# Optimization experiments

Measured on AMD Instinct MI355X. Metric: run time of the kernel, lower is better.

Reference implementation:

```python
import jax, jax.numpy as jnp
import numpy as np

B, S, D, U = 4, 2048, 1024, 1024

def setup_inputs() -> dict:
    key = jax.random.key(0)
    ks = jax.random.split(key, 6)
    glorot = lambda k, shape: jax.random.uniform(k, shape, jnp.float32,
                                                 -np.sqrt(6.0/(shape[0]+shape[1])),
                                                 np.sqrt(6.0/(shape[0]+shape[1])))
    return {
        "inputs": jax.random.normal(ks[0], (B, S, D), jnp.float32),
        "Wq": glorot(ks[1], (D, U)),
        "Wk": glorot(ks[2], (D, U)),
        "Wv": glorot(ks[3], (D, U)),
        "Wo": glorot(ks[4], (U, D)),
        "bo": jnp.zeros((D,), jnp.float32),
        "scale": jnp.asarray(1.0 / np.sqrt(U), jnp.float32),
    }

def reference(inputs, Wq, Wk, Wv, Wo, bo, scale):
    # q, k, v: [B, S, U]
    q = jnp.einsum('bsd,du->bsu', inputs, Wq)
    k = jnp.einsum('bsd,du->bsu', inputs, Wk)
    v = jnp.einsum('bsd,du->bsu', inputs, Wv)
    # scores: [B, S, S]
    scores = jnp.einsum('bqu,bku->bqk', q, k) * scale
    weights = jax.nn.softmax(scores, axis=-1)
    context = jnp.einsum('bqk,bku->bqu', weights, v)
    output = jnp.einsum('bsu,ud->bsd', context, Wo) + bo
    return (output, weights)
```

## Files before the change

### kernel.cpp

```cpp
#include <hip/hip_runtime.h>
#include <hip/hip_bf16.h>

#define BB 4
#define SS 2048
#define DD 1024
#define UU 1024
#define NTOK (BB*SS)

typedef unsigned short ushort_t;
typedef __attribute__((ext_vector_type(8))) short bf16x8;
typedef __attribute__((ext_vector_type(4))) float f32x4;
typedef __attribute__((ext_vector_type(4))) unsigned short u16x4;

__device__ inline unsigned short f2bf(float f) {
  unsigned u = __builtin_bit_cast(unsigned, f);
  u += 0x7FFFu + ((u >> 16) & 1u);
  return (unsigned short)(u >> 16);
}

__device__ inline void gload_lds16(const ushort_t* g, ushort_t* l) {
  __builtin_amdgcn_global_load_lds(
      (const __attribute__((address_space(1))) void*)g,
      (__attribute__((address_space(3))) void*)l, 16, 0, 0);
}

#define WAIT_LGKM0 do { asm volatile("s_waitcnt lgkmcnt(0)" ::: "memory"); \
                        __builtin_amdgcn_sched_barrier(0); } while(0)
#define WAIT_VM(N) do { asm volatile("s_waitcnt vmcnt(" #N ")" ::: "memory"); \
                        __builtin_amdgcn_sched_barrier(0); } while(0)
#define BAR        do { __builtin_amdgcn_s_barrier(); \
                        __builtin_amdgcn_sched_barrier(0); } while(0)

__global__ __launch_bounds__(256) void cast_f32_bf16(const float* __restrict__ in,
                                                     ushort_t* __restrict__ out,
                                                     long n) {
  long i = ((long)blockIdx.x * blockDim.x + threadIdx.x) * 4;
  long stride = (long)gridDim.x * blockDim.x * 4;
  for (long idx = i; idx < n; idx += stride) {
    float4 v = *(const float4*)(in + idx);
    u16x4 o;
    o[0] = f2bf(v.x); o[1] = f2bf(v.y); o[2] = f2bf(v.z); o[3] = f2bf(v.w);
    *(u16x4*)(out + idx) = o;
  }
}

struct TPack { const float* s[4]; ushort_t* d[4]; };
__global__ __launch_bounds__(256) void transpose_cast_w4(TPack p) {
  __shared__ float tile[32][33];
  const float* in = p.s[blockIdx.z];
  ushort_t* out = p.d[blockIdx.z];
  int bx = blockIdx.x * 32, by = blockIdx.y * 32;
  int tx = threadIdx.x, ty = threadIdx.y;
  #pragma unroll
  for (int j = 0; j < 32; j += 8)
    tile[ty + j][tx] = in[(long)(by + ty + j) * 1024 + bx + tx];
  __syncthreads();
  #pragma unroll
  for (int j = 0; j < 32; j += 8)
    out[(long)(bx + ty + j) * 1024 + by + tx] = f2bf(tile[tx][ty + j]);
}

__global__ __launch_bounds__(256) void transpose_bf16_batched(const ushort_t* __restrict__ in,
                                                              ushort_t* __restrict__ out,
                                                              int R, int C) {
  __shared__ ushort_t tile[32][34];
  long z = (long)blockIdx.z * R * C;
  int bx = blockIdx.x * 32, by = blockIdx.y * 32;
  int tx = threadIdx.x, ty = threadIdx.y;
  #pragma unroll
  for (int j = 0; j < 32; j += 8)
    tile[ty + j][tx] = in[z + (long)(by + ty + j) * C + bx + tx];
  __syncthreads();
  #pragma unroll
  for (int j = 0; j < 32; j += 8)
    out[z + (long)(bx + ty + j) * R + by + tx] = tile[tx][ty + j];
}

template<int BN>
__global__ __launch_bounds__(512, 2) void gemm8p(
    const ushort_t* __restrict__ A,
    const ushort_t* __restrict__ Bt,
    float* __restrict__ Cf,
    ushort_t* __restrict__ Cb,
    const float* __restrict__ bias,
    const float* __restrict__ alpha_ptr,
    int M, int N, int K,
    long sA, long sB, long sC) {
  static_assert(BN == 128 || BN == 256, "BN");
  constexpr int NREP = BN / 64;
  constexpr int BSTEPS = BN / 64;
  __shared__ __align__(16) ushort_t As[2][256 * 64];
  __shared__ __align__(16) ushort_t Bs[2][BN * 64];

  const int tid = threadIdx.x;
  const int lane = tid & 63;
  const int wid = tid >> 6;
  const int wm = wid >> 2, wn = wid & 3;

  int bx = blockIdx.x, by = blockIdx.y, bz = blockIdx.z;
  {
    const int gx = gridDim.x, gy = gridDim.y, gz = gridDim.z;
    const int total = gx * gy * gz;
    const int ppx = total >> 3;
    if ((total & 7) == 0 && ppx % gx == 0) {
      const int lin = blockIdx.x + gx * (blockIdx.y + gy * blockIdx.z);
      const int xcd = lin & 7, i = lin >> 3;
      const int p = xcd * (ppx / gx) + i / gx;
      bx = i % gx; by = p % gy; bz = p / gy;
    }
  }

  const long zA = (long)bz * sA;
  const long zB = (long)bz * sB;
  const long zC = (long)bz * sC;
  const int m0 = by * 256;
  const int n0 = bx * BN;

  f32x4 acc[8][NREP] = {};

  const int srow = tid >> 3;
  const int cs = (tid & 7) ^ (srow & 7);
  const ushort_t* Aps = A + zA + (long)(m0 + srow) * K + cs * 8;
  const ushort_t* Bps = Bt + zB + (long)(n0 + srow) * K + cs * 8;
  const int ldst = wid * 512;

  const int rsel = (lane & 15);
  const int csel = (lane >> 4);
  const int cxor = (lane & 7);

  const int nt = K / 64;

  auto STAGE = [&](int tk, int b) {
    const long kof = (long)tk * 64;
    #pragma unroll
    for (int j = 0; j < BSTEPS; ++j)
      gload_lds16(Bps + (long)(j * 64) * K + kof, &Bs[b][j * 4096 + ldst]);
    gload_lds16(Aps + (long)(0 * 64) * K + kof, &As[b][0 * 4096 + ldst]);
    gload_lds16(Aps + (long)(2 * 64) * K + kof, &As[b][2 * 4096 + ldst]);
    gload_lds16(Aps + (long)(1 * 64) * K + kof, &As[b][1 * 4096 + ldst]);
    gload_lds16(Aps + (long)(3 * 64) * K + kof, &As[b][3 * 4096 + ldst]);
  };

  STAGE(0, 0);
  WAIT_VM(2);
  BAR;

  for (int t = 0; t < nt; ++t) {
    const int cur = t & 1, nxt = cur ^ 1;
    const bool pf = (t + 1 < nt);
    const ushort_t* __restrict__ Ac = &As[cur][0];
    const ushort_t* __restrict__ Bc = &Bs[cur][0];

    bf16x8 bfr[NREP][2], af[4][2];

    #pragma unroll
    for (int n = 0; n < NREP; ++n)
      #pragma unroll
      for (int kk = 0; kk < 2; ++kk)
        bfr[n][kk] = *(const bf16x8*)&Bc[(wn * (BN/4) + n * 16 + rsel) * 64
                                         + ((kk * 4 + csel) ^ cxor) * 8];
    #pragma unroll
    for (int m = 0; m < 4; ++m)
      #pragma unroll
      for (int kk = 0; kk < 2; ++kk)
        af[m][kk] = *(const bf16x8*)&Ac[(wm * 128 + m * 16 + rsel) * 64
                                        + ((kk * 4 + csel) ^ cxor) * 8];
    if (pf) STAGE(t + 1, nxt);
    BAR;
    WAIT_LGKM0;
    __builtin_amdgcn_s_setprio(1);
    #pragma unroll
    for (int m = 0; m < 4; ++m)
      #pragma unroll
      for (int n = 0; n < (NREP == 4 ? 2 : NREP); ++n)
        #pragma unroll
        for (int kk = 0; kk < 2; ++kk)
          acc[m][n] = __builtin_amdgcn_mfma_f32_16x16x32_bf16(af[m][kk], bfr[n][kk], acc[m][n], 0, 0, 0);
    __builtin_amdgcn_s_setprio(0);
    BAR;

    if (NREP == 4) {
      __builtin_amdgcn_s_setprio(1);
      #pragma unroll
      for (int m = 0; m < 4; ++m)
        #pragma unroll
        for (int n = 2; n < 4; ++n)
          #pragma unroll
          for (int kk = 0; kk < 2; ++kk)
            acc[m][n] = __builtin_amdgcn_mfma_f32_16x16x32_bf16(af[m][kk], bfr[n][kk], acc[m][n], 0, 0, 0);
      __builtin_amdgcn_s_setprio(0);
      if (pf) { WAIT_VM(8); } else { WAIT_VM(0); }
      BAR;

      #pragma unroll
      for (int m = 0; m < 4; ++m)
        #pragma unroll
        for (int kk = 0; kk < 2; ++kk)
          af[m][kk] = *(const bf16x8*)&Ac[(wm * 128 + 64 + m * 16 + rsel) * 64
                                          + ((kk * 4 + csel) ^ cxor) * 8];
      BAR;
      WAIT_LGKM0;
      __builtin_amdgcn_s_setprio(1);
      #pragma unroll
      for (int m = 0; m < 4; ++m)
        #pragma unroll
        for (int n = 0; n < 2; ++n)
          #pragma unroll
          for (int kk = 0; kk < 2; ++kk)
            acc[m + 4][n] = __builtin_amdgcn_mfma_f32_16x16x32_bf16(af[m][kk], bfr[n][kk], acc[m + 4][n], 0, 0, 0);
      __builtin_amdgcn_s_setprio(0);
      BAR;

      __builtin_amdgcn_s_setprio(1);
      #pragma unroll
      for (int m = 0; m < 4; ++m)
        #pragma unroll
        for (int n = 2; n < 4; ++n)
          #pragma unroll
          for (int kk = 0; kk < 2; ++kk)
            acc[m + 4][n] = __builtin_amdgcn_mfma_f32_16x16x32_bf16(af[m][kk], bfr[n][kk], acc[m + 4][n], 0, 0, 0);
      __builtin_amdgcn_s_setprio(0);
      if (pf) { WAIT_VM(2); }
      BAR;
    } else {
      if (pf) { WAIT_VM(6); } else { WAIT_VM(0); }
      BAR;

      #pragma unroll
      for (int m = 0; m < 4; ++m)
        #pragma unroll
        for (int kk = 0; kk < 2; ++kk)
          af[m][kk] = *(const bf16x8*)&Ac[(wm * 128 + 64 + m * 16 + rsel) * 64
                                          + ((kk * 4 + csel) ^ cxor) * 8];
      BAR;
      WAIT_LGKM0;
      __builtin_amdgcn_s_setprio(1);
      #pragma unroll
      for (int m = 0; m < 4; ++m)
        #pragma unroll
        for (int n = 0; n < NREP; ++n)
          #pragma unroll
          for (int kk = 0; kk < 2; ++kk)
            acc[m + 4][n] = __builtin_amdgcn_mfma_f32_16x16x32_bf16(af[m][kk], bfr[n][kk], acc[m + 4][n], 0, 0, 0);
      __builtin_amdgcn_s_setprio(0);
      if (pf) { WAIT_VM(2); }
      BAR;
    }
  }

  const float alpha = alpha_ptr ? *alpha_ptr : 1.0f;
  const int crow0 = m0 + wm * 128 + csel * 4;
  const int ccol0 = n0 + wn * (BN / 4) + rsel;
  #pragma unroll
  for (int m = 0; m < 8; ++m) {
    #pragma unroll
    for (int n = 0; n < NREP; ++n) {
      const int cc = ccol0 + n * 16;
      const float bv = bias ? bias[cc] : 0.0f;
      #pragma unroll
      for (int r = 0; r < 4; ++r) {
        const int rr = crow0 + m * 16 + r;
        const float v = acc[m][n][r] * alpha + bv;
        const long idx = zC + (long)rr * N + cc;
        if (Cf) Cf[idx] = v;
        if (Cb) Cb[idx] = f2bf(v);
      }
    }
  }
}

__global__ __launch_bounds__(256) void softmax_rows(float* __restrict__ Wf,
                                                    ushort_t* __restrict__ Pb) {
  const int t = threadIdx.x;
  const int lane = t & 63, wid = t >> 6;
  const long base = (long)blockIdx.x * SS;
  float* p = Wf + base;

  float4 a = *(const float4*)(p + t * 4);
  float4 b = *(const float4*)(p + 1024 + t * 4);

  float m = fmaxf(fmaxf(fmaxf(a.x, a.y), fmaxf(a.z, a.w)),
                  fmaxf(fmaxf(b.x, b.y), fmaxf(b.z, b.w)));
  #pragma unroll
  for (int off = 32; off; off >>= 1) m = fmaxf(m, __shfl_xor(m, off));
  __shared__ float redm[4];
  __shared__ float reds[4];
  if (lane == 0) redm[wid] = m;
  __syncthreads();
  m = fmaxf(fmaxf(redm[0], redm[1]), fmaxf(redm[2], redm[3]));

  float e[8];
  e[0] = __expf(a.x - m); e[1] = __expf(a.y - m); e[2] = __expf(a.z - m); e[3] = __expf(a.w - m);
  e[4] = __expf(b.x - m); e[5] = __expf(b.y - m); e[6] = __expf(b.z - m); e[7] = __expf(b.w - m);
  float s = (e[0] + e[1]) + (e[2] + e[3]) + (e[4] + e[5]) + (e[6] + e[7]);
  #pragma unroll
  for (int off = 32; off; off >>= 1) s += __shfl_xor(s, off);
  if (lane == 0) reds[wid] = s;
  __syncthreads();
  s = (reds[0] + reds[1]) + (reds[2] + reds[3]);
  const float inv = 1.0f / s;

  float4 oa = make_float4(e[0] * inv, e[1] * inv, e[2] * inv, e[3] * inv);
  float4 ob = make_float4(e[4] * inv, e[5] * inv, e[6] * inv, e[7] * inv);
  *(float4*)(p + t * 4) = oa;
  *(float4*)(p + 1024 + t * 4) = ob;

  u16x4 ba, bb2;
  ba[0] = f2bf(oa.x); ba[1] = f2bf(oa.y); ba[2] = f2bf(oa.z); ba[3] = f2bf(oa.w);
  bb2[0] = f2bf(ob.x); bb2[1] = f2bf(ob.y); bb2[2] = f2bf(ob.z); bb2[3] = f2bf(ob.w);
  *(u16x4*)(Pb + base + t * 4) = ba;
  *(u16x4*)(Pb + base + 1024 + t * 4) = bb2;
}

extern "C" void kernel_launch(void* const* d_in, const int* in_sizes, int n_in,
                              void* d_out, int out_size, void* d_ws, size_t ws_size,
                              hipStream_t stream) {
  const float* X     = (const float*)d_in[0];
  const float* Wq    = (const float*)d_in[1];
  const float* Wk    = (const float*)d_in[2];
  const float* Wv    = (const float*)d_in[3];
  const float* Wo    = (const float*)d_in[4];
  const float* bo    = (const float*)d_in[5];
  const float* scale = (const float*)d_in[6];

  float* out = (float*)d_out;
  float* wts = out + (long)NTOK * DD;

  ushort_t* ws = (ushort_t*)d_ws;
  ushort_t* Xb  = ws;
  ushort_t* Qb  = Xb + (long)NTOK * DD;
  ushort_t* Kb  = Qb + (long)NTOK * UU;
  ushort_t* Vb  = Kb + (long)NTOK * UU;
  ushort_t* Wqt = Vb + (long)NTOK * UU;
  ushort_t* Wkt = Wqt + (long)UU * DD;
  ushort_t* Wvt = Wkt + (long)UU * DD;
  ushort_t* Wot = Wvt + (long)UU * DD;
  ushort_t* Cb  = Xb;
  ushort_t* Vt  = Qb;
  ushort_t* Pb  = Kb;

  cast_f32_bf16<<<2048, 256, 0, stream>>>(X, Xb, (long)NTOK * DD);

  TPack tp;
  tp.s[0] = Wq; tp.s[1] = Wk; tp.s[2] = Wv; tp.s[3] = Wo;
  tp.d[0] = Wqt; tp.d[1] = Wkt; tp.d[2] = Wvt; tp.d[3] = Wot;
  transpose_cast_w4<<<dim3(32, 32, 4), dim3(32, 8), 0, stream>>>(tp);

  dim3 gProj(UU/128, NTOK/256, 3);
  gemm8p<128><<<gProj, 512, 0, stream>>>(Xb, Wqt, nullptr, Qb, nullptr, nullptr,
                                         NTOK, UU, DD,
                                         0, (long)UU * DD, (long)NTOK * UU);

  dim3 gScores(SS/256, SS/256, BB);
  gemm8p<256><<<gScores, 512, 0, stream>>>(Qb, Kb, wts, nullptr, nullptr, scale,
                                           SS, SS, UU,
                                           (long)SS * UU, (long)SS * UU, (long)SS * SS);

  transpose_bf16_batched<<<dim3(UU/32, SS/32, BB), dim3(32, 8), 0, stream>>>(Vb, Vt, SS, UU);

  softmax_rows<<<BB * SS, 256, 0, stream>>>(wts, Pb);

  dim3 gPV(UU/128, SS/256, BB);
  gemm8p<128><<<gPV, 512, 0, stream>>>(Pb, Vt, nullptr, Cb, nullptr, nullptr,
                                       SS, UU, SS,
                                       (long)SS * SS, (long)UU * SS, (long)SS * UU);

  dim3 gOut(DD/128, NTOK/256, 1);
  gemm8p<128><<<gOut, 512, 0, stream>>>(Cb, Wot, out, nullptr, bo, nullptr,
                                        NTOK, DD, UU, 0, 0, 0);
}
```

Before: 361.1 us.

## Split GEMM into 256x256 and 128x256 kernels with two-tile unrolled pipelines

Replaces the templated GEMM with two kernels. One is a 256x256 kernel that processes two K-tiles per iteration and staggers A and B prefetches across the compute phases. The other is a 128x256 kernel with a triple-buffered B tile in LDS. The projection GEMM moves to 256-wide N tiles, and the PV and output GEMMs move to 128x256 tiles. The goal is to overlap global-to-LDS loads with MFMA phases more finely and to raise data reuse, at the cost of more LDS per block and more complex waitcnt accounting that could race if the counts are wrong.

```diff
diff --git a/kernel.cpp b/kernel.cpp
--- a/kernel.cpp
+++ b/kernel.cpp
@@ -26,10 +26,14 @@
 
 #define WAIT_LGKM0 do { asm volatile("s_waitcnt lgkmcnt(0)" ::: "memory"); \
                         __builtin_amdgcn_sched_barrier(0); } while(0)
+#define WAIT_LGKM(N) do { asm volatile("s_waitcnt lgkmcnt(" #N ")" ::: "memory"); \
+                        __builtin_amdgcn_sched_barrier(0); } while(0)
 #define WAIT_VM(N) do { asm volatile("s_waitcnt vmcnt(" #N ")" ::: "memory"); \
                         __builtin_amdgcn_sched_barrier(0); } while(0)
 #define BAR        do { __builtin_amdgcn_s_barrier(); \
                         __builtin_amdgcn_sched_barrier(0); } while(0)
+#define PRIO1      __builtin_amdgcn_s_setprio(1)
+#define PRIO0      __builtin_amdgcn_s_setprio(0)
 
 __global__ __launch_bounds__(256) void cast_f32_bf16(const float* __restrict__ in,
                                                      ushort_t* __restrict__ out,
@@ -76,8 +80,27 @@
     out[z + (long)(bx + ty + j) * R + by + tx] = tile[tx][ty + j];
 }
 
-template<int BN>
-__global__ __launch_bounds__(512, 2) void gemm8p(
+#define RD_A(Ax, MB) do { \
+  _Pragma("unroll") for (int m = 0; m < 4; ++m) \
+    _Pragma("unroll") for (int kk = 0; kk < 2; ++kk) \
+      af[m][kk] = *(const bf16x8*)&(Ax)[((MB) + m * 16 + rsel) * 64 \
+                                        + ((kk * 4 + csel) ^ cxor) * 8]; \
+} while(0)
+#define RD_B(Bx, NH) do { \
+  _Pragma("unroll") for (int n = 0; n < 2; ++n) \
+    _Pragma("unroll") for (int kk = 0; kk < 2; ++kk) \
+      bfr[(NH)*2 + n][kk] = *(const bf16x8*)&(Bx)[(wn * 64 + ((NH)*2 + n) * 16 + rsel) * 64 \
+                                                  + ((kk * 4 + csel) ^ cxor) * 8]; \
+} while(0)
+#define MM16(MH, NH) do { \
+  _Pragma("unroll") for (int m = 0; m < 4; ++m) \
+    _Pragma("unroll") for (int n = 0; n < 2; ++n) \
+      _Pragma("unroll") for (int kk = 0; kk < 2; ++kk) \
+        acc[(MH)*4 + m][(NH)*2 + n] = __builtin_amdgcn_mfma_f32_16x16x32_bf16( \
+            af[m][kk], bfr[(NH)*2 + n][kk], acc[(MH)*4 + m][(NH)*2 + n], 0, 0, 0); \
+} while(0)
+
+__global__ __launch_bounds__(512, 2) void gemm256_8p(
     const ushort_t* __restrict__ A,
     const ushort_t* __restrict__ Bt,
     float* __restrict__ Cf,
@@ -86,11 +109,8 @@
     const float* __restrict__ alpha_ptr,
     int M, int N, int K,
     long sA, long sB, long sC) {
-  static_assert(BN == 128 || BN == 256, "BN");
-  constexpr int NREP = BN / 64;
-  constexpr int BSTEPS = BN / 64;
   __shared__ __align__(16) ushort_t As[2][256 * 64];
-  __shared__ __align__(16) ushort_t Bs[2][BN * 64];
+  __shared__ __align__(16) ushort_t Bs[2][256 * 64];
 
   const int tid = threadIdx.x;
   const int lane = tid & 63;
@@ -114,9 +134,9 @@
   const long zB = (long)bz * sB;
   const long zC = (long)bz * sC;
   const int m0 = by * 256;
-  const int n0 = bx * BN;
-
-  f32x4 acc[8][NREP] = {};
+  const int n0 = bx * 256;
+
+  f32x4 acc[8][4] = {};
 
   const int srow = tid >> 3;
   const int cs = (tid & 7) ^ (srow & 7);
@@ -129,132 +149,89 @@
   const int cxor = (lane & 7);
 
   const int nt = K / 64;
-
-  auto STAGE = [&](int tk, int b) {
-    const long kof = (long)tk * 64;
-    #pragma unroll
-    for (int j = 0; j < BSTEPS; ++j)
-      gload_lds16(Bps + (long)(j * 64) * K + kof, &Bs[b][j * 4096 + ldst]);
-    gload_lds16(Aps + (long)(0 * 64) * K + kof, &As[b][0 * 4096 + ldst]);
-    gload_lds16(Aps + (long)(2 * 64) * K + kof, &As[b][2 * 4096 + ldst]);
-    gload_lds16(Aps + (long)(1 * 64) * K + kof, &As[b][1 * 4096 + ldst]);
-    gload_lds16(Aps + (long)(3 * 64) * K + kof, &As[b][3 * 4096 + ldst]);
-  };
-
-  STAGE(0, 0);
-  WAIT_VM(2);
+  const int nIter = nt / 2;
+
+  #define STA256(tk, g) gload_lds16(Aps + (long)((g) * 64) * K + (long)(tk) * 64, \
+                                    &As[(tk) & 1][(g) * 4096 + ldst])
+  #define STB256(tk, g) gload_lds16(Bps + (long)((g) * 64) * K + (long)(tk) * 64, \
+                                    &Bs[(tk) & 1][(g) * 4096 + ldst])
+
+  STB256(0, 0); STB256(0, 1); STB256(0, 2); STB256(0, 3);
+  STA256(0, 0); STA256(0, 1); STA256(0, 2); STA256(0, 3);
+  STB256(1, 0); STB256(1, 1); STB256(1, 2); STB256(1, 3);
+  WAIT_VM(4);
   BAR;
 
-  for (int t = 0; t < nt; ++t) {
-    const int cur = t & 1, nxt = cur ^ 1;
-    const bool pf = (t + 1 < nt);
-    const ushort_t* __restrict__ Ac = &As[cur][0];
-    const ushort_t* __restrict__ Bc = &Bs[cur][0];
-
-    bf16x8 bfr[NREP][2], af[4][2];
-
-    #pragma unroll
-    for (int n = 0; n < NREP; ++n)
-      #pragma unroll
-      for (int kk = 0; kk < 2; ++kk)
-        bfr[n][kk] = *(const bf16x8*)&Bc[(wn * (BN/4) + n * 16 + rsel) * 64
-                                         + ((kk * 4 + csel) ^ cxor) * 8];
-    #pragma unroll
-    for (int m = 0; m < 4; ++m)
-      #pragma unroll
-      for (int kk = 0; kk < 2; ++kk)
-        af[m][kk] = *(const bf16x8*)&Ac[(wm * 128 + m * 16 + rsel) * 64
-                                        + ((kk * 4 + csel) ^ cxor) * 8];
-    if (pf) STAGE(t + 1, nxt);
-    BAR;
-    WAIT_LGKM0;
-    __builtin_amdgcn_s_setprio(1);
-    #pragma unroll
-    for (int m = 0; m < 4; ++m)
-      #pragma unroll
-      for (int n = 0; n < (NREP == 4 ? 2 : NREP); ++n)
-        #pragma unroll
-        for (int kk = 0; kk < 2; ++kk)
-          acc[m][n] = __builtin_amdgcn_mfma_f32_16x16x32_bf16(af[m][kk], bfr[n][kk], acc[m][n], 0, 0, 0);
-    __builtin_amdgcn_s_setprio(0);
-    BAR;
-
-    if (NREP == 4) {
-      __builtin_amdgcn_s_setprio(1);
-      #pragma unroll
-      for (int m = 0; m < 4; ++m)
-        #pragma unroll
-        for (int n = 2; n < 4; ++n)
-          #pragma unroll
-          for (int kk = 0; kk < 2; ++kk)
-            acc[m][n] = __builtin_amdgcn_mfma_f32_16x16x32_bf16(af[m][kk], bfr[n][kk], acc[m][n], 0, 0, 0);
-      __builtin_amdgcn_s_setprio(0);
-      if (pf) { WAIT_VM(8); } else { WAIT_VM(0); }
-      BAR;
-
-      #pragma unroll
-      for (int m = 0; m < 4; ++m)
-        #pragma unroll
-        for (int kk = 0; kk < 2; ++kk)
-          af[m][kk] = *(const bf16x8*)&Ac[(wm * 128 + 64 + m * 16 + rsel) * 64
-                                          + ((kk * 4 + csel) ^ cxor) * 8];
-      BAR;
-      WAIT_LGKM0;
-      __builtin_amdgcn_s_setprio(1);
-      #pragma unroll
-      for (int m = 0; m < 4; ++m)
-        #pragma unroll
-        for (int n = 0; n < 2; ++n)
-          #pragma unroll
-          for (int kk = 0; kk < 2; ++kk)
-            acc[m + 4][n] = __builtin_amdgcn_mfma_f32_16x16x32_bf16(af[m][kk], bfr[n][kk], acc[m + 4][n], 0, 0, 0);
-      __builtin_amdgcn_s_setprio(0);
-      BAR;
-
-      __builtin_amdgcn_s_setprio(1);
-      #pragma unroll
-      for (int m = 0; m < 4; ++m)
-        #pragma unroll
-        for (int n = 2; n < 4; ++n)
-          #pragma unroll
-          for (int kk = 0; kk < 2; ++kk)
-            acc[m + 4][n] = __builtin_amdgcn_mfma_f32_16x16x32_bf16(af[m][kk], bfr[n][kk], acc[m + 4][n], 0, 0, 0);
-      __builtin_amdgcn_s_setprio(0);
-      if (pf) { WAIT_VM(2); }
-      BAR;
-    } else {
-      if (pf) { WAIT_VM(6); } else { WAIT_VM(0); }
-      BAR;
-
-      #pragma unroll
-      for (int m = 0; m < 4; ++m)
-        #pragma unroll
-        for (int kk = 0; kk < 2; ++kk)
-          af[m][kk] = *(const bf16x8*)&Ac[(wm * 128 + 64 + m * 16 + rsel) * 64
-                                          + ((kk * 4 + csel) ^ cxor) * 8];
-      BAR;
-      WAIT_LGKM0;
-      __builtin_amdgcn_s_setprio(1);
-      #pragma unroll
-      for (int m = 0; m < 4; ++m)
-        #pragma unroll
-        for (int n = 0; n < NREP; ++n)
-          #pragma unroll
-          for (int kk = 0; kk < 2; ++kk)
-            acc[m + 4][n] = __builtin_amdgcn_mfma_f32_16x16x32_bf16(af[m][kk], bfr[n][kk], acc[m + 4][n], 0, 0, 0);
-      __builtin_amdgcn_s_setprio(0);
-      if (pf) { WAIT_VM(2); }
-      BAR;
-    }
+  for (int it = 0; it < nIter; ++it) {
+    const int E = 2 * it, O = E + 1;
+    const bool pf = (it + 1 < nIter);
+    const ushort_t* __restrict__ Ae = &As[0][0];
+    const ushort_t* __restrict__ Be = &Bs[0][0];
+    const ushort_t* __restrict__ Ao = &As[1][0];
+    const ushort_t* __restrict__ Bo = &Bs[1][0];
+
+    bf16x8 af[4][2], bfr[4][2];
+
+    RD_A(Ae, wm * 128);
+    RD_B(Be, 0);
+    STA256(O, 0); STA256(O, 1);
+    WAIT_LGKM(8);
+    BAR; WAIT_LGKM0;
+    PRIO1; MM16(0, 0); PRIO0;
+    BAR;
+
+    RD_B(Be, 1);
+    STA256(O, 2); STA256(O, 3);
+    BAR; WAIT_LGKM0;
+    PRIO1; MM16(0, 1); PRIO0;
+    BAR;
+
+    RD_A(Ae, wm * 128 + 64);
+    if (pf) { STB256(E + 2, 0); STB256(E + 2, 1); }
+    BAR; WAIT_LGKM0;
+    PRIO1; MM16(1, 0); PRIO0;
+    BAR;
+
+    if (pf) { STB256(E + 2, 2); STB256(E + 2, 3); }
+    BAR;
+    PRIO1; MM16(1, 1); PRIO0;
+    if (pf) { WAIT_VM(4); } else { WAIT_VM(0); }
+    BAR;
+
+    RD_A(Ao, wm * 128);
+    RD_B(Bo, 0);
+    if (pf) { STA256(E + 2, 0); STA256(E + 2, 1); }
+    WAIT_LGKM(8);
+    BAR; WAIT_LGKM0;
+    PRIO1; MM16(0, 0); PRIO0;
+    BAR;
+
+    RD_B(Bo, 1);
+    if (pf) { STA256(E + 2, 2); STA256(E + 2, 3); }
+    BAR; WAIT_LGKM0;
+    PRIO1; MM16(0, 1); PRIO0;
+    BAR;
+
+    RD_A(Ao, wm * 128 + 64);
+    if (pf) { STB256(O + 2, 0); STB256(O + 2, 1); }
+    BAR; WAIT_LGKM0;
+    PRIO1; MM16(1, 0); PRIO0;
+    BAR;
+
+    if (pf) { STB256(O + 2, 2); STB256(O + 2, 3); }
+    BAR;
+    PRIO1; MM16(1, 1); PRIO0;
+    if (pf) { WAIT_VM(4); } else { WAIT_VM(0); }
+    BAR;
   }
 
   const float alpha = alpha_ptr ? *alpha_ptr : 1.0f;
   const int crow0 = m0 + wm * 128 + csel * 4;
-  const int ccol0 = n0 + wn * (BN / 4) + rsel;
+  const int ccol0 = n0 + wn * 64 + rsel;
   #pragma unroll
   for (int m = 0; m < 8; ++m) {
     #pragma unroll
-    for (int n = 0; n < NREP; ++n) {
+    for (int n = 0; n < 4; ++n) {
       const int cc = ccol0 + n * 16;
       const float bv = bias ? bias[cc] : 0.0f;
       #pragma unroll
@@ -267,6 +244,135 @@
       }
     }
   }
+  #undef STA256
+  #undef STB256
+}
+
+__global__ __launch_bounds__(512, 2) void gemm128_4p(
+    const ushort_t* __restrict__ A,
+    const ushort_t* __restrict__ Bt,
+    float* __restrict__ Cf,
+    ushort_t* __restrict__ Cb,
+    const float* __restrict__ bias,
+    const float* __restrict__ alpha_ptr,
+    int M, int N, int K,
+    long sA, long sB, long sC) {
+  __shared__ __align__(16) ushort_t As[2][128 * 64];
+  __shared__ __align__(16) ushort_t Bs[3][256 * 64];
+
+  const int tid = threadIdx.x;
+  const int lane = tid & 63;
+  const int wid = tid >> 6;
+  const int wm = wid >> 2, wn = wid & 3;
+
+  int bx = blockIdx.x, by = blockIdx.y, bz = blockIdx.z;
+  {
+    const int gx = gridDim.x, gy = gridDim.y, gz = gridDim.z;
+    const int total = gx * gy * gz;
+    const int ppx = total >> 3;
+    if ((total & 7) == 0 && ppx % gx == 0) {
+      const int lin = blockIdx.x + gx * (blockIdx.y + gy * blockIdx.z);
+      const int xcd = lin & 7, i = lin >> 3;
+      const int p = xcd * (ppx / gx) + i / gx;
+      bx = i % gx; by = p % gy; bz = p / gy;
+    }
+  }
+
+  const long zA = (long)bz * sA;
+  const long zB = (long)bz * sB;
+  const long zC = (long)bz * sC;
+  const int m0 = by * 128;
+  const int n0 = bx * 256;
+
+  f32x4 acc[4][4] = {};
+
+  const int srow = tid >> 3;
+  const int cs = (tid & 7) ^ (srow & 7);
+  const ushort_t* Aps = A + zA + (long)(m0 + srow) * K + cs * 8;
+  const ushort_t* Bps = Bt + zB + (long)(n0 + srow) * K + cs * 8;
+  const int ldst = wid * 512;
+
+  const int rsel = (lane & 15);
+  const int csel = (lane >> 4);
+  const int cxor = (lane & 7);
+
+  const int nt = K / 64;
+  const int nIter = nt / 2;
+
+  #define STA128(tk, g) gload_lds16(Aps + (long)((g) * 64) * K + (long)(tk) * 64, \
+                                    &As[(tk) & 1][(g) * 4096 + ldst])
+  #define STB128(tk, g) gload_lds16(Bps + (long)((g) * 64) * K + (long)(tk) * 64, \
+                                    &Bs[(tk) % 3][(g) * 4096 + ldst])
+
+  STB128(0, 0); STB128(0, 1); STB128(0, 2); STB128(0, 3);
+  STA128(0, 0); STA128(0, 1);
+  STB128(1, 0); STB128(1, 1); STB128(1, 2); STB128(1, 3);
+  STA128(1, 0); STA128(1, 1);
+  WAIT_VM(6);
+  BAR;
+
+  for (int it = 0; it < nIter; ++it) {
+    const int E = 2 * it, O = E + 1;
+    const bool pf = (it + 1 < nIter);
+    const ushort_t* __restrict__ Ae = &As[0][0];
+    const ushort_t* __restrict__ Ao = &As[1][0];
+    const ushort_t* __restrict__ Be = &Bs[E % 3][0];
+    const ushort_t* __restrict__ Bo = &Bs[O % 3][0];
+
+    bf16x8 af[4][2], bfr[4][2];
+
+    RD_A(Ae, wm * 64);
+    RD_B(Be, 0);
+    if (pf) { STB128(E + 2, 0); STB128(E + 2, 1); }
+    WAIT_LGKM(8);
+    BAR; WAIT_LGKM0;
+    PRIO1; MM16(0, 0); PRIO0;
+    BAR;
+
+    RD_B(Be, 1);
+    if (pf) { STB128(E + 2, 2); STB128(E + 2, 3); STA128(E + 2, 0); STA128(E + 2, 1); }
+    BAR; WAIT_LGKM0;
+    PRIO1; MM16(0, 1); PRIO0;
+    if (pf) { WAIT_VM(6); } else { WAIT_VM(0); }
+    BAR;
+
+    RD_A(Ao, wm * 64);
+    RD_B(Bo, 0);
+    if (pf) { STB128(O + 2, 0); STB128(O + 2, 1); }
+    WAIT_LGKM(8);
+    BAR; WAIT_LGKM0;
+    PRIO1; MM16(0, 0); PRIO0;
+    BAR;
+
+    RD_B(Bo, 1);
+    if (pf) { STB128(O + 2, 2); STB128(O + 2, 3); STA128(O + 2, 0); STA128(O + 2, 1); }
+    BAR; WAIT_LGKM0;
+    PRIO1; MM16(0, 1); PRIO0;
+    if (pf) { WAIT_VM(6); } else { WAIT_VM(0); }
+    BAR;
+  }
+
+  const float alpha = alpha_ptr ? *alpha_ptr : 1.0f;
+  const int crow0 = m0 + wm * 64 + csel * 4;
+  const int ccol0 = n0 + wn * 64 + rsel;
+  #pragma unroll
+  for (int m = 0; m < 4; ++m) {
+    #pragma unroll
+    for (int n = 0; n < 4; ++n) {
+      const int cc = ccol0 + n * 16;
+      const float bv = bias ? bias[cc] : 0.0f;
+      #pragma unroll
+      for (int r = 0; r < 4; ++r) {
+        const int rr = crow0 + m * 16 + r;
+        const float v = acc[m][n][r] * alpha + bv;
+        const long idx = zC + (long)rr * N + cc;
+        if (Cf) Cf[idx] = v;
+        if (Cb) Cb[idx] = f2bf(v);
+      }
+    }
+  }
+  #undef STA128
+  #undef STB128
 }
 
 __global__ __launch_bounds__(256) void softmax_rows(float* __restrict__ Wf,
@@ -346,26 +452,26 @@
   tp.d[0] = Wqt; tp.d[1] = Wkt; tp.d[2] = Wvt; tp.d[3] = Wot;
   transpose_cast_w4<<<dim3(32, 32, 4), dim3(32, 8), 0, stream>>>(tp);
 
-  dim3 gProj(UU/128, NTOK/256, 3);
-  gemm8p<128><<<gProj, 512, 0, stream>>>(Xb, Wqt, nullptr, Qb, nullptr, nullptr,
-                                         NTOK, UU, DD,
-                                         0, (long)UU * DD, (long)NTOK * UU);
+  dim3 gProj(UU/256, NTOK/256, 3);
+  gemm256_8p<<<gProj, 512, 0, stream>>>(Xb, Wqt, nullptr, Qb, nullptr, nullptr,
+                                        NTOK, UU, DD,
+                                        0, (long)UU * DD, (long)NTOK * UU);
 
   dim3 gScores(SS/256, SS/256, BB);
-  gemm8p<256><<<gScores, 512, 0, stream>>>(Qb, Kb, wts, nullptr, nullptr, scale,
-                                           SS, SS, UU,
-                                           (long)SS * UU, (long)SS * UU, (long)SS * SS);
+  gemm256_8p<<<gScores, 512, 0, stream>>>(Qb, Kb, wts, nullptr, nullptr, scale,
+                                          SS, SS, UU,
+                                          (long)SS * UU, (long)SS * UU, (long)SS * SS);
 
   transpose_bf16_batched<<<dim3(UU/32, SS/32, BB), dim3(32, 8), 0, stream>>>(Vb, Vt, SS, UU);
 
   softmax_rows<<<BB * SS, 256, 0, stream>>>(wts, Pb);
 
-  dim3 gPV(UU/128, SS/256, BB);
-  gemm8p<128><<<gPV, 512, 0, stream>>>(Pb, Vt, nullptr, Cb, nullptr, nullptr,
-                                       SS, UU, SS,
-                                       (long)SS * SS, (long)UU * SS, (long)SS * UU);
-
-  dim3 gOut(DD/128, NTOK/256, 1);
-  gemm8p<128><<<gOut, 512, 0, stream>>>(Cb, Wot, out, nullptr, bo, nullptr,
-                                        NTOK, DD, UU, 0, 0, 0);
-}
+  dim3 gPV(UU/256, SS/128, BB);
+  gemm128_4p<<<gPV, 512, 0, stream>>>(Pb, Vt, nullptr, Cb, nullptr, nullptr,
+                                      SS, UU, SS,
+                                      (long)SS * SS, (long)UU * SS, (long)SS * UU);
+
+  dim3 gOut(DD/256, NTOK/128, 1);
+  gemm128_4p<<<gOut, 512, 0, stream>>>(Cb, Wot, out, nullptr, bo, nullptr,
+                                       NTOK, DD, UU, 0, 0, 0);
+}
```

New measurement: 347.1 us. -3.9%, faster.
